# Optimization experiments

Measured on AMD Instinct MI355X. Metric: run time of the kernel, lower is better.

Reference implementation:

```python
import jax, jax.numpy as jnp
import numpy as np

B, T, C, H = 4, 2048, 768, 12
D = C // H

def setup_inputs() -> dict:
    key = jax.random.key(0)
    ks = jax.random.split(key, 8)
    s = 1.0 / np.sqrt(C)
    return {
        "x":  jax.random.normal(ks[0], (B, T, C), dtype=jnp.float32),
        "Wq": jax.random.normal(ks[1], (C, C), dtype=jnp.float32) * s,
        "bq": jax.random.normal(ks[2], (C,), dtype=jnp.float32) * 0.02,
        "Wk": jax.random.normal(ks[3], (C, C), dtype=jnp.float32) * s,
        "bk": jax.random.normal(ks[4], (C,), dtype=jnp.float32) * 0.02,
        "Wv": jax.random.normal(ks[5], (C, C), dtype=jnp.float32) * s,
        "bv": jax.random.normal(ks[6], (C,), dtype=jnp.float32) * 0.02,
        "Wp": jax.random.normal(ks[7], (C, C), dtype=jnp.float32) * s,
    }

def reference(x, Wq, bq, Wk, bk, Wv, bv, Wp):
    # Linear projections (torch Linear: y = x @ W.T + b)
    q = x @ Wq.T + bq
    k = x @ Wk.T + bk
    v = x @ Wv.T + bv
    # [B,T,C] -> [B,H,T,D]
    q = q.reshape(B, T, H, D).transpose(0, 2, 1, 3)
    k = k.reshape(B, T, H, D).transpose(0, 2, 1, 3)
    v = v.reshape(B, T, H, D).transpose(0, 2, 1, 3)
    scale = 1.0 / np.sqrt(D).astype(np.float32)
    scores = jnp.einsum('bhqd,bhkd->bhqk', q, k) * scale  # [B,H,T,T]
    attn = jax.nn.softmax(scores, axis=-1)  # no mask in original module
    out = jnp.einsum('bhqk,bhkd->bhqd', attn, v)
    out = out.transpose(0, 2, 1, 3).reshape(B, T, C)
    return out @ Wp.T  # proj has bias=False
```

## Files before the change

### kernel.cpp

```cpp
#include <hip/hip_runtime.h>
#include <hip/hip_bf16.h>
#include <cmath>

constexpr int B  = 4;
constexpr int T  = 2048;
constexpr int C  = 768;
constexpr int H  = 12;
constexpr int Dh = 64;
constexpr int M  = B * T;
constexpr int NQKV = 3 * C;
constexpr int WS2  = C * C;

typedef short bf16x8 __attribute__((ext_vector_type(8)));
typedef short bf16x4 __attribute__((ext_vector_type(4)));
typedef float f32x4  __attribute__((ext_vector_type(4)));

__device__ inline short f2bf(float f) {
    unsigned u = __float_as_uint(f);
    u += 0x7fffu + ((u >> 16) & 1u);
    return (short)(u >> 16);
}

__device__ inline unsigned pk_bf16(float a, float b) {
    __hip_bfloat162 h = __float22bfloat162_rn(float2{a, b});
    return *(unsigned*)&h;
}

typedef const __attribute__((address_space(1))) unsigned GU;
typedef __attribute__((address_space(3))) unsigned LU;
__device__ inline void async_copy16(const void* g, void* l) {
    __builtin_amdgcn_global_load_lds((GU*)g, (LU*)l, 16, 0, 0);
}

constexpr size_t XE = (size_t)M * C;
constexpr size_t CV_TOTAL = XE + 4 * (size_t)WS2;

__global__ __launch_bounds__(256)
void convert_all(const float* __restrict__ x,  const float* __restrict__ Wq,
                 const float* __restrict__ Wk, const float* __restrict__ Wv,
                 const float* __restrict__ Wp,
                 short* __restrict__ xb, short* __restrict__ Wqkv,
                 short* __restrict__ Wpb) {
    size_t i = ((size_t)blockIdx.x * 256 + threadIdx.x) * 4;
    const float* src; short* dst; size_t off;
    if (i < XE)                        { src = x;  dst = xb;            off = i; }
    else if (i < XE + WS2)             { src = Wq; dst = Wqkv;          off = i - XE; }
    else if (i < XE + 2 * (size_t)WS2) { src = Wk; dst = Wqkv + WS2;    off = i - XE - WS2; }
    else if (i < XE + 3 * (size_t)WS2) { src = Wv; dst = Wqkv + 2 * WS2; off = i - XE - 2 * (size_t)WS2; }
    else                               { src = Wp; dst = Wpb;           off = i - XE - 3 * (size_t)WS2; }
    float4 v = *(const float4*)(src + off);
    bf16x4 o; o[0] = f2bf(v.x); o[1] = f2bf(v.y); o[2] = f2bf(v.z); o[3] = f2bf(v.w);
    *(bf16x4*)(dst + off) = o;
}

constexpr int BM = 128;

template<int BN_, int WMW, int WNW, int OUT_BF16>
__global__ __launch_bounds__(256)
void gemm_bt(const short* __restrict__ A, const short* __restrict__ W,
             const float* __restrict__ bias0, const float* __restrict__ bias1,
             const float* __restrict__ bias2,
             void* __restrict__ Yv, int Ndim, int Kdim) {
    constexpr int MT  = BM / WMW / 16;
    constexpr int NT  = BN_ / WNW / 16;
    constexpr int NCH = (BM + BN_) / 16;

    __shared__ short As[2][BM * 32];
    __shared__ short Bs[2][BN_ * 32];

    const int tid  = threadIdx.x;
    const int wave = tid >> 6;
    const int lane = tid & 63;
    const int li   = lane & 15;
    const int quad = lane >> 4;
    const int wm   = wave % WMW;
    const int wn   = wave / WMW;
    const int m0   = blockIdx.y * BM;
    const int n0   = blockIdx.x * BN_;

    f32x4 acc[MT][NT];
    #pragma unroll
    for (int i = 0; i < MT; ++i)
        #pragma unroll
        for (int j = 0; j < NT; ++j)
            acc[i][j] = (f32x4){0.f, 0.f, 0.f, 0.f};

    const int lrow = lane >> 2;
    const int lkof = (lane & 3) * 8;

    auto stage = [&](int kk, int pbuf) {
        #pragma unroll
        for (int ii = 0; ii < NCH / 4; ++ii) {
            int c = ii * 4 + wave;
            if (c < BM / 16)
                async_copy16(A + (size_t)(m0 + c * 16 + lrow) * Kdim + kk + lkof,
                             &As[pbuf][c * 512]);
            else
                async_copy16(W + (size_t)(n0 + (c - BM / 16) * 16 + lrow) * Kdim + kk + lkof,
                             &Bs[pbuf][(c - BM / 16) * 512]);
        }
    };

    stage(0, 0);

    int pi = 0;
    for (int k0 = 0; k0 < Kdim; k0 += 32, pi ^= 1) {
        __syncthreads();
        if (k0 + 32 < Kdim) stage(k0 + 32, pi ^ 1);

        bf16x8 af[MT], bfr[NT];
        #pragma unroll
        for (int t = 0; t < MT; ++t)
            af[t] = *(const bf16x8*)&As[pi][(wm * MT * 16 + t * 16 + li) * 32 + quad * 8];
        #pragma unroll
        for (int t = 0; t < NT; ++t)
            bfr[t] = *(const bf16x8*)&Bs[pi][(wn * NT * 16 + t * 16 + li) * 32 + quad * 8];
        #pragma unroll
        for (int i = 0; i < MT; ++i)
            #pragma unroll
            for (int j = 0; j < NT; ++j)
                acc[i][j] = __builtin_amdgcn_mfma_f32_16x16x32_bf16(
                    af[i], bfr[j], acc[i][j], 0, 0, 0);
    }

    float bb[NT];
    #pragma unroll
    for (int nt = 0; nt < NT; ++nt) bb[nt] = 0.f;
    if (bias0) {
        int s = n0 / C;
        const float* bp = (s == 0) ? bias0 : ((s == 1) ? bias1 : bias2);
        int nb = n0 % C;
        #pragma unroll
        for (int nt = 0; nt < NT; ++nt)
            bb[nt] = bp[nb + wn * NT * 16 + nt * 16 + li];
    }

    #pragma unroll
    for (int mt = 0; mt < MT; ++mt)
        #pragma unroll
        for (int nt = 0; nt < NT; ++nt)
            #pragma unroll
            for (int r = 0; r < 4; ++r) {
                int row = m0 + wm * MT * 16 + mt * 16 + quad * 4 + r;
                int col = n0 + wn * NT * 16 + nt * 16 + li;
                float v = acc[mt][nt][r] + bb[nt];
                if constexpr (OUT_BF16)
                    ((short*)Yv)[(size_t)row * Ndim + col] = f2bf(v);
                else
                    ((float*)Yv)[(size_t)row * Ndim + col] = v;
            }
}

constexpr int QT    = 128;
constexpr int KTT   = 32;
constexpr int KHALF = T / 2;
constexpr int KSTR  = 72;
constexpr int VSTR  = 40;
constexpr int PSTR  = 40;
constexpr int QS    = NQKV;
constexpr float SOFT_SCALE = 0.18033688011112042f;

__global__ __launch_bounds__(256)
void attn_fwd(const short* __restrict__ QKV, float* __restrict__ Opart,
              float* __restrict__ Lpart) {
    __shared__ short Ks[KTT * KSTR];
    __shared__ short Vt[Dh * VSTR];
    __shared__ short Ps[4 * 32 * PSTR];

    const int tid  = threadIdx.x;
    const int wave = tid >> 6;
    const int lane = tid & 63;
    const int li   = lane & 15;
    const int quad = lane >> 4;
    const int half = blockIdx.z & 1;
    const int b    = blockIdx.z >> 1;
    const int h    = blockIdx.y;
    const int qw   = blockIdx.x * QT + wave * 32;
    const int kt0  = half * KHALF;

    const short* Qg = QKV + (size_t)(b * T) * QS + h * Dh;
    const short* Kg = QKV + (size_t)(b * T) * QS + C + h * Dh;
    const short* Vg = QKV + (size_t)(b * T) * QS + 2 * C + h * Dh;

    bf16x8 qf[2][2];
    #pragma unroll
    for (int qb = 0; qb < 2; ++qb)
        #pragma unroll
        for (int dh = 0; dh < 2; ++dh)
            qf[qb][dh] = *(const bf16x8*)(Qg + (size_t)(qw + qb * 16 + li) * QS
                                             + dh * 32 + quad * 8);

    bf16x8 ones;
    #pragma unroll
    for (int i = 0; i < 8; ++i) ones[i] = (short)0x3F80;

    f32x4 oacc[2][4];
    #pragma unroll
    for (int qb = 0; qb < 2; ++qb)
        #pragma unroll
        for (int db = 0; db < 4; ++db)
            oacc[qb][db] = (f32x4){0.f, 0.f, 0.f, 0.f};
    f32x4 lacc[2] = {(f32x4){0.f, 0.f, 0.f, 0.f}, (f32x4){0.f, 0.f, 0.f, 0.f}};

    const int ktok = tid >> 3;
    const int kch  = tid & 7;
    const int vd2  = (tid & 31) * 2;
    const int vg   = tid >> 5;

    int4 kpre;
    unsigned vpre[4];
    kpre = *(const int4*)(Kg + (size_t)(kt0 + ktok) * QS + kch * 8);
    #pragma unroll
    for (int t2 = 0; t2 < 4; ++t2)
        vpre[t2] = *(const unsigned*)(Vg + (size_t)(kt0 + vg * 4 + t2) * QS + vd2);

    for (int kt = kt0; kt < kt0 + KHALF; kt += KTT) {
        __syncthreads();

        *(int4*)&Ks[ktok * KSTR + kch * 8] = kpre;
        {
            unsigned lo0 = __builtin_amdgcn_perm(vpre[1], vpre[0], 0x05040100u);
            unsigned lo1 = __builtin_amdgcn_perm(vpre[3], vpre[2], 0x05040100u);
            unsigned hi0 = __builtin_amdgcn_perm(vpre[1], vpre[0], 0x07060302u);
            unsigned hi1 = __builtin_amdgcn_perm(vpre[3], vpre[2], 0x07060302u);
            *(uint2*)&Vt[vd2 * VSTR + vg * 4]       = make_uint2(lo0, lo1);
            *(uint2*)&Vt[(vd2 + 1) * VSTR + vg * 4] = make_uint2(hi0, hi1);
        }
        __syncthreads();

        if (kt + KTT < kt0 + KHALF) {
            const size_t nb = kt + KTT;
            kpre = *(const int4*)(Kg + (nb + ktok) * QS + kch * 8);
            #pragma unroll
            for (int t2 = 0; t2 < 4; ++t2)
                vpre[t2] = *(const unsigned*)(Vg + (nb + vg * 4 + t2) * QS + vd2);
        }

        f32x4 st[2][2];
        #pragma unroll
        for (int kb = 0; kb < 2; ++kb) {
            bf16x8 kf0 = *(const bf16x8*)&Ks[(kb * 16 + li) * KSTR + quad * 8];
            bf16x8 kf1 = *(const bf16x8*)&Ks[(kb * 16 + li) * KSTR + 32 + quad * 8];
            #pragma unroll
            for (int qb = 0; qb < 2; ++qb) {
                f32x4 a = (f32x4){0.f, 0.f, 0.f, 0.f};
                a = __builtin_amdgcn_mfma_f32_16x16x32_bf16(kf0, qf[qb][0], a, 0, 0, 0);
                a = __builtin_amdgcn_mfma_f32_16x16x32_bf16(kf1, qf[qb][1], a, 0, 0, 0);
                st[qb][kb] = a;
            }
        }

        #pragma unroll
        for (int qb = 0; qb < 2; ++qb)
            #pragma unroll
            for (int kb = 0; kb < 2; ++kb) {
                float p0 = __builtin_amdgcn_exp2f(st[qb][kb][0] * SOFT_SCALE);
                float p1 = __builtin_amdgcn_exp2f(st[qb][kb][1] * SOFT_SCALE);
                float p2 = __builtin_amdgcn_exp2f(st[qb][kb][2] * SOFT_SCALE);
                float p3 = __builtin_amdgcn_exp2f(st[qb][kb][3] * SOFT_SCALE);
                uint2 w; w.x = pk_bf16(p0, p1); w.y = pk_bf16(p2, p3);
                *(uint2*)&Ps[(wave * 32 + qb * 16 + li) * PSTR + kb * 16 + quad * 4] = w;
            }
        __asm__ volatile("s_waitcnt lgkmcnt(0)" ::: "memory");

        bf16x8 pf[2];
        #pragma unroll
        for (int qb = 0; qb < 2; ++qb) {
            pf[qb] = *(const bf16x8*)&Ps[(wave * 32 + qb * 16 + li) * PSTR + quad * 8];
            lacc[qb] = __builtin_amdgcn_mfma_f32_16x16x32_bf16(
                pf[qb], ones, lacc[qb], 0, 0, 0);
        }
        #pragma unroll
        for (int db = 0; db < 4; ++db) {
            bf16x8 vf = *(const bf16x8*)&Vt[(db * 16 + li) * VSTR + quad * 8];
            #pragma unroll
            for (int qb = 0; qb < 2; ++qb)
                oacc[qb][db] = __builtin_amdgcn_mfma_f32_16x16x32_bf16(
                    pf[qb], vf, oacc[qb][db], 0, 0, 0);
        }
    }

    float* Ob = Opart + (size_t)half * M * C;
    #pragma unroll
    for (int qb = 0; qb < 2; ++qb)
        #pragma unroll
        for (int r = 0; r < 4; ++r) {
            int row = qw + qb * 16 + quad * 4 + r;
            float* op = Ob + ((size_t)(b * T) + row) * C + h * Dh + li;
            #pragma unroll
            for (int db = 0; db < 4; ++db)
                op[db * 16] = oacc[qb][db][r];
            if (li == 0)
                Lpart[(size_t)half * M * H + ((size_t)(b * T) + row) * H + h]
                    = lacc[qb][r];
        }
}

__global__ __launch_bounds__(256)
void attn_reduce(const float* __restrict__ Op, const float* __restrict__ Lp,
                 short* __restrict__ AO) {
    int i = (blockIdx.x * 256 + threadIdx.x) * 8;
    int row = i / C;
    int col = i % C;
    int h = col >> 6;
    float l = Lp[(size_t)row * H + h] + Lp[(size_t)M * H + (size_t)row * H + h];
    float inv = 1.0f / l;
    const float* p0 = Op + i;
    const float* p1 = Op + (size_t)M * C + i;
    float4 a0 = *(const float4*)(p0);
    float4 a1 = *(const float4*)(p0 + 4);
    float4 b0 = *(const float4*)(p1);
    float4 b1 = *(const float4*)(p1 + 4);
    bf16x8 o;
    o[0] = f2bf((a0.x + b0.x) * inv); o[1] = f2bf((a0.y + b0.y) * inv);
    o[2] = f2bf((a0.z + b0.z) * inv); o[3] = f2bf((a0.w + b0.w) * inv);
    o[4] = f2bf((a1.x + b1.x) * inv); o[5] = f2bf((a1.y + b1.y) * inv);
    o[6] = f2bf((a1.z + b1.z) * inv); o[7] = f2bf((a1.w + b1.w) * inv);
    *(bf16x8*)(AO + i) = o;
}

extern "C" void kernel_launch(void* const* d_in, const int* in_sizes, int n_in,
                              void* d_out, int out_size, void* d_ws, size_t ws_size,
                              hipStream_t stream) {
    (void)in_sizes; (void)n_in; (void)out_size; (void)ws_size;

    const float* x  = (const float*)d_in[0];
    const float* Wq = (const float*)d_in[1];
    const float* bq = (const float*)d_in[2];
    const float* Wk = (const float*)d_in[3];
    const float* bk = (const float*)d_in[4];
    const float* Wv = (const float*)d_in[5];
    const float* bv = (const float*)d_in[6];
    const float* Wp = (const float*)d_in[7];
    float* out = (float*)d_out;

    short* xb    = (short*)d_ws;
    short* Wqkv  = xb + XE;
    short* Wpb   = Wqkv + 3 * (size_t)WS2;
    short* QKVb  = Wpb + (size_t)WS2;
    float* Opart = (float*)(QKVb + (size_t)M * NQKV);
    float* Lpart = (float*)Wqkv;
    short* AOb   = xb;

    convert_all<<<dim3(CV_TOTAL / 1024), 256, 0, stream>>>(
        x, Wq, Wk, Wv, Wp, xb, Wqkv, Wpb);

    gemm_bt<128, 2, 2, 1><<<dim3(NQKV / 128, M / BM), 256, 0, stream>>>(
        xb, Wqkv, bq, bk, bv, QKVb, NQKV, C);

    attn_fwd<<<dim3(T / QT, H, B * 2), 256, 0, stream>>>(QKVb, Opart, Lpart);

    attn_reduce<<<dim3((M * C) / 2048), 256, 0, stream>>>(Opart, Lpart, AOb);

    gemm_bt<64, 4, 1, 0><<<dim3(C / 64, M / BM), 256, 0, stream>>>(
        AOb, Wpb, nullptr, nullptr, nullptr, out, C, C);
}
```

Measured before the change: 250.1 us.

## Keep P in registers via 16x16x16 MFMA, sum rows in VALU, store partials as bf16

The attention kernel no longer writes the probability tile to LDS and reads it back. The exp outputs are packed directly into bf16x4 operands for 16x16x16 MFMAs against V, which removes the LDS round trip, the wait, and the ones-vector MFMA for row sums. Row sums are now accumulated in fp32 per lane and reduced with cross-lane shuffles. Partial outputs are stored as bf16 instead of fp32, halving partial-output traffic in both attention and reduce, at the cost of extra rounding error and twice as many smaller MFMAs.

```diff
diff --git a/kernel.cpp b/kernel.cpp
--- a/kernel.cpp
+++ b/kernel.cpp
@@ -156,16 +156,14 @@
 constexpr int KHALF = T / 2;
 constexpr int KSTR  = 72;
 constexpr int VSTR  = 40;
-constexpr int PSTR  = 40;
 constexpr int QS    = NQKV;
 constexpr float SOFT_SCALE = 0.18033688011112042f;
 
 __global__ __launch_bounds__(256)
-void attn_fwd(const short* __restrict__ QKV, float* __restrict__ Opart,
+void attn_fwd(const short* __restrict__ QKV, short* __restrict__ Opart,
               float* __restrict__ Lpart) {
     __shared__ short Ks[KTT * KSTR];
     __shared__ short Vt[Dh * VSTR];
-    __shared__ short Ps[4 * 32 * PSTR];
 
     const int tid  = threadIdx.x;
     const int wave = tid >> 6;
@@ -190,17 +188,13 @@
             qf[qb][dh] = *(const bf16x8*)(Qg + (size_t)(qw + qb * 16 + li) * QS
                                              + dh * 32 + quad * 8);
 
-    bf16x8 ones;
-    #pragma unroll
-    for (int i = 0; i < 8; ++i) ones[i] = (short)0x3F80;
-
     f32x4 oacc[2][4];
     #pragma unroll
     for (int qb = 0; qb < 2; ++qb)
         #pragma unroll
         for (int db = 0; db < 4; ++db)
             oacc[qb][db] = (f32x4){0.f, 0.f, 0.f, 0.f};
-    f32x4 lacc[2] = {(f32x4){0.f, 0.f, 0.f, 0.f}, (f32x4){0.f, 0.f, 0.f, 0.f}};
+    float lpart[2] = {0.f, 0.f};
 
     const int ktok = tid >> 3;
     const int kch  = tid & 7;
@@ -250,6 +244,7 @@
             }
         }
 
+        bf16x4 pf[2][2];
         #pragma unroll
         for (int qb = 0; qb < 2; ++qb)
             #pragma unroll
@@ -258,46 +253,55 @@
                 float p1 = __builtin_amdgcn_exp2f(st[qb][kb][1] * SOFT_SCALE);
                 float p2 = __builtin_amdgcn_exp2f(st[qb][kb][2] * SOFT_SCALE);
                 float p3 = __builtin_amdgcn_exp2f(st[qb][kb][3] * SOFT_SCALE);
-                uint2 w; w.x = pk_bf16(p0, p1); w.y = pk_bf16(p2, p3);
-                *(uint2*)&Ps[(wave * 32 + qb * 16 + li) * PSTR + kb * 16 + quad * 4] = w;
+                lpart[qb] += (p0 + p1) + (p2 + p3);
+                unsigned w0 = pk_bf16(p0, p1), w1 = pk_bf16(p2, p3);
+                uint2 packed = make_uint2(w0, w1);
+                pf[qb][kb] = *(bf16x4*)&packed;
             }
-        __asm__ volatile("s_waitcnt lgkmcnt(0)" ::: "memory");
-
-        bf16x8 pf[2];
-        #pragma unroll
-        for (int qb = 0; qb < 2; ++qb) {
-            pf[qb] = *(const bf16x8*)&Ps[(wave * 32 + qb * 16 + li) * PSTR + quad * 8];
-            lacc[qb] = __builtin_amdgcn_mfma_f32_16x16x32_bf16(
-                pf[qb], ones, lacc[qb], 0, 0, 0);
-        }
-        #pragma unroll
-        for (int db = 0; db < 4; ++db) {
-            bf16x8 vf = *(const bf16x8*)&Vt[(db * 16 + li) * VSTR + quad * 8];
-            #pragma unroll
-            for (int qb = 0; qb < 2; ++qb)
-                oacc[qb][db] = __builtin_amdgcn_mfma_f32_16x16x32_bf16(
-                    pf[qb], vf, oacc[qb][db], 0, 0, 0);
-        }
-    }
-
-    float* Ob = Opart + (size_t)half * M * C;
+
+        #pragma unroll
+        for (int kb = 0; kb < 2; ++kb)
+            #pragma unroll
+            for (int db = 0; db < 4; ++db) {
+                bf16x4 vf = *(const bf16x4*)&Vt[(db * 16 + li) * VSTR
+                                                + kb * 16 + quad * 4];
+                #pragma unroll
+                for (int qb = 0; qb < 2; ++qb)
+                    oacc[qb][db] = __builtin_amdgcn_mfma_f32_16x16x16bf16_1k(
+                        pf[qb][kb], vf, oacc[qb][db], 0, 0, 0);
+            }
+    }
+
+    float lq[2];
+    #pragma unroll
+    for (int qb = 0; qb < 2; ++qb) {
+        float v = lpart[qb];
+        v += __shfl_xor(v, 16);
+        v += __shfl_xor(v, 32);
+        lq[qb] = v;
+    }
+    if (quad == 0) {
+        #pragma unroll
+        for (int qb = 0; qb < 2; ++qb)
+            Lpart[(size_t)half * M * H + ((size_t)(b * T) + qw + qb * 16 + li) * H + h]
+                = lq[qb];
+    }
+
+    short* Ob = Opart + (size_t)half * M * C;
     #pragma unroll
     for (int qb = 0; qb < 2; ++qb)
         #pragma unroll
         for (int r = 0; r < 4; ++r) {
             int row = qw + qb * 16 + quad * 4 + r;
-            float* op = Ob + ((size_t)(b * T) + row) * C + h * Dh + li;
+            short* op = Ob + ((size_t)(b * T) + row) * C + h * Dh + li;
             #pragma unroll
             for (int db = 0; db < 4; ++db)
-                op[db * 16] = oacc[qb][db][r];
-            if (li == 0)
-                Lpart[(size_t)half * M * H + ((size_t)(b * T) + row) * H + h]
-                    = lacc[qb][r];
+                op[db * 16] = f2bf(oacc[qb][db][r]);
         }
 }
 
 __global__ __launch_bounds__(256)
-void attn_reduce(const float* __restrict__ Op, const float* __restrict__ Lp,
+void attn_reduce(const short* __restrict__ Op, const float* __restrict__ Lp,
                  short* __restrict__ AO) {
     int i = (blockIdx.x * 256 + threadIdx.x) * 8;
     int row = i / C;
@@ -305,17 +309,20 @@
     int h = col >> 6;
     float l = Lp[(size_t)row * H + h] + Lp[(size_t)M * H + (size_t)row * H + h];
     float inv = 1.0f / l;
-    const float* p0 = Op + i;
-    const float* p1 = Op + (size_t)M * C + i;
-    float4 a0 = *(const float4*)(p0);
-    float4 a1 = *(const float4*)(p0 + 4);
-    float4 b0 = *(const float4*)(p1);
-    float4 b1 = *(const float4*)(p1 + 4);
+    uint4 a = *(const uint4*)(Op + i);
+    uint4 bq = *(const uint4*)(Op + (size_t)M * C + i);
+    const unsigned* au = &a.x;
+    const unsigned* bu = &bq.x;
     bf16x8 o;
-    o[0] = f2bf((a0.x + b0.x) * inv); o[1] = f2bf((a0.y + b0.y) * inv);
-    o[2] = f2bf((a0.z + b0.z) * inv); o[3] = f2bf((a0.w + b0.w) * inv);
-    o[4] = f2bf((a1.x + b1.x) * inv); o[5] = f2bf((a1.y + b1.y) * inv);
-    o[6] = f2bf((a1.z + b1.z) * inv); o[7] = f2bf((a1.w + b1.w) * inv);
+    #pragma unroll
+    for (int j = 0; j < 4; ++j) {
+        float alo = __uint_as_float(au[j] << 16);
+        float ahi = __uint_as_float(au[j] & 0xffff0000u);
+        float blo = __uint_as_float(bu[j] << 16);
+        float bhi = __uint_as_float(bu[j] & 0xffff0000u);
+        o[2 * j]     = f2bf((alo + blo) * inv);
+        o[2 * j + 1] = f2bf((ahi + bhi) * inv);
+    }
     *(bf16x8*)(AO + i) = o;
 }
 
@@ -338,7 +345,7 @@
     short* Wqkv  = xb + XE;
     short* Wpb   = Wqkv + 3 * (size_t)WS2;
     short* QKVb  = Wpb + (size_t)WS2;
-    float* Opart = (float*)(QKVb + (size_t)M * NQKV);
+    short* Opart = QKVb + (size_t)M * NQKV;
     float* Lpart = (float*)Wqkv;
     short* AOb   = xb;
 
```

New measurement: 253.3 us. Within noise of the previous version (+1.3%).

## Use register-prefetch GEMM staging with BK=64 and bf16 attention partials

Applied to the files above, without the earlier changes.

The GEMM drops the async global-to-LDS double buffer. It now prefetches the next 64-wide K slice into registers, writes it to a single LDS buffer between two barriers, and runs two MFMA k-steps per tile. Separately, the split-K attention partial outputs are stored as bf16 instead of fp32, which halves the write and read traffic of the partials in attn_fwd and attn_reduce. The risks are more barriers per K step, more register pressure from the prefetch buffers, possible LDS bank conflicts with the unpadded 64-wide rows, and extra rounding error from bf16 partial sums.

```diff
diff --git a/kernel.cpp b/kernel.cpp
--- a/kernel.cpp
+++ b/kernel.cpp
@@ -24,12 +24,6 @@
 __device__ inline unsigned pk_bf16(float a, float b) {
     __hip_bfloat162 h = __float22bfloat162_rn(float2{a, b});
     return *(unsigned*)&h;
-}
-
-typedef const __attribute__((address_space(1))) unsigned GU;
-typedef __attribute__((address_space(3))) unsigned LU;
-__device__ inline void async_copy16(const void* g, void* l) {
-    __builtin_amdgcn_global_load_lds((GU*)g, (LU*)l, 16, 0, 0);
 }
 
 constexpr size_t XE = (size_t)M * C;
@@ -63,10 +57,11 @@
              void* __restrict__ Yv, int Ndim, int Kdim) {
     constexpr int MT  = BM / WMW / 16;
     constexpr int NT  = BN_ / WNW / 16;
-    constexpr int NCH = (BM + BN_) / 16;
-
-    __shared__ short As[2][BM * 32];
-    __shared__ short Bs[2][BN_ * 32];
+    constexpr int CHA = BM / 32;
+    constexpr int CHW = BN_ / 32;
+
+    __shared__ short As[BM * 64];
+    __shared__ short Bs[BN_ * 64];
 
     const int tid  = threadIdx.x;
     const int wave = tid >> 6;
@@ -85,42 +80,54 @@
         for (int j = 0; j < NT; ++j)
             acc[i][j] = (f32x4){0.f, 0.f, 0.f, 0.f};
 
-    const int lrow = lane >> 2;
-    const int lkof = (lane & 3) * 8;
-
-    auto stage = [&](int kk, int pbuf) {
-        #pragma unroll
-        for (int ii = 0; ii < NCH / 4; ++ii) {
-            int c = ii * 4 + wave;
-            if (c < BM / 16)
-                async_copy16(A + (size_t)(m0 + c * 16 + lrow) * Kdim + kk + lkof,
-                             &As[pbuf][c * 512]);
-            else
-                async_copy16(W + (size_t)(n0 + (c - BM / 16) * 16 + lrow) * Kdim + kk + lkof,
-                             &Bs[pbuf][(c - BM / 16) * 512]);
-        }
+    const int srow = tid >> 3;
+    const int sch  = (tid & 7) * 8;
+
+    const short* Abase = A + (size_t)(m0 + srow) * Kdim + sch;
+    const short* Wbase = W + (size_t)(n0 + srow) * Kdim + sch;
+
+    int4 pre[CHA + CHW];
+    auto prefetch = [&](int kk) {
+        #pragma unroll
+        for (int i = 0; i < CHA; ++i)
+            pre[i] = *(const int4*)(Abase + (size_t)i * 32 * Kdim + kk);
+        #pragma unroll
+        for (int i = 0; i < CHW; ++i)
+            pre[CHA + i] = *(const int4*)(Wbase + (size_t)i * 32 * Kdim + kk);
     };
-
-    stage(0, 0);
-
-    int pi = 0;
-    for (int k0 = 0; k0 < Kdim; k0 += 32, pi ^= 1) {
+    prefetch(0);
+
+    short* Adst = &As[srow * 64 + sch];
+    short* Wdst = &Bs[srow * 64 + sch];
+
+    for (int k0 = 0; k0 < Kdim; k0 += 64) {
         __syncthreads();
-        if (k0 + 32 < Kdim) stage(k0 + 32, pi ^ 1);
-
-        bf16x8 af[MT], bfr[NT];
-        #pragma unroll
-        for (int t = 0; t < MT; ++t)
-            af[t] = *(const bf16x8*)&As[pi][(wm * MT * 16 + t * 16 + li) * 32 + quad * 8];
-        #pragma unroll
-        for (int t = 0; t < NT; ++t)
-            bfr[t] = *(const bf16x8*)&Bs[pi][(wn * NT * 16 + t * 16 + li) * 32 + quad * 8];
-        #pragma unroll
-        for (int i = 0; i < MT; ++i)
-            #pragma unroll
-            for (int j = 0; j < NT; ++j)
-                acc[i][j] = __builtin_amdgcn_mfma_f32_16x16x32_bf16(
-                    af[i], bfr[j], acc[i][j], 0, 0, 0);
+        #pragma unroll
+        for (int i = 0; i < CHA; ++i) *(int4*)(Adst + i * 2048) = pre[i];
+        #pragma unroll
+        for (int i = 0; i < CHW; ++i) *(int4*)(Wdst + i * 2048) = pre[CHA + i];
+        __syncthreads();
+
+        if (k0 + 64 < Kdim) prefetch(k0 + 64);
+
+        #pragma unroll
+        for (int h = 0; h < 2; ++h) {
+            bf16x8 af[MT], bfr[NT];
+            #pragma unroll
+            for (int t = 0; t < MT; ++t)
+                af[t] = *(const bf16x8*)&As[(wm * MT * 16 + t * 16 + li) * 64
+                                            + h * 32 + quad * 8];
+            #pragma unroll
+            for (int t = 0; t < NT; ++t)
+                bfr[t] = *(const bf16x8*)&Bs[(wn * NT * 16 + t * 16 + li) * 64
+                                             + h * 32 + quad * 8];
+            #pragma unroll
+            for (int i = 0; i < MT; ++i)
+                #pragma unroll
+                for (int j = 0; j < NT; ++j)
+                    acc[i][j] = __builtin_amdgcn_mfma_f32_16x16x32_bf16(
+                        af[i], bfr[j], acc[i][j], 0, 0, 0);
+        }
     }
 
     float bb[NT];
@@ -161,7 +168,7 @@
 constexpr float SOFT_SCALE = 0.18033688011112042f;
 
 __global__ __launch_bounds__(256)
-void attn_fwd(const short* __restrict__ QKV, float* __restrict__ Opart,
+void attn_fwd(const short* __restrict__ QKV, short* __restrict__ Opart,
               float* __restrict__ Lpart) {
     __shared__ short Ks[KTT * KSTR];
     __shared__ short Vt[Dh * VSTR];
@@ -280,16 +287,16 @@
         }
     }
 
-    float* Ob = Opart + (size_t)half * M * C;
+    short* Ob = Opart + (size_t)half * M * C;
     #pragma unroll
     for (int qb = 0; qb < 2; ++qb)
         #pragma unroll
         for (int r = 0; r < 4; ++r) {
             int row = qw + qb * 16 + quad * 4 + r;
-            float* op = Ob + ((size_t)(b * T) + row) * C + h * Dh + li;
+            short* op = Ob + ((size_t)(b * T) + row) * C + h * Dh + li;
             #pragma unroll
             for (int db = 0; db < 4; ++db)
-                op[db * 16] = oacc[qb][db][r];
+                op[db * 16] = f2bf(oacc[qb][db][r]);
             if (li == 0)
                 Lpart[(size_t)half * M * H + ((size_t)(b * T) + row) * H + h]
                     = lacc[qb][r];
@@ -297,7 +304,7 @@
 }
 
 __global__ __launch_bounds__(256)
-void attn_reduce(const float* __restrict__ Op, const float* __restrict__ Lp,
+void attn_reduce(const short* __restrict__ Op, const float* __restrict__ Lp,
                  short* __restrict__ AO) {
     int i = (blockIdx.x * 256 + threadIdx.x) * 8;
     int row = i / C;
@@ -305,17 +312,20 @@
     int h = col >> 6;
     float l = Lp[(size_t)row * H + h] + Lp[(size_t)M * H + (size_t)row * H + h];
     float inv = 1.0f / l;
-    const float* p0 = Op + i;
-    const float* p1 = Op + (size_t)M * C + i;
-    float4 a0 = *(const float4*)(p0);
-    float4 a1 = *(const float4*)(p0 + 4);
-    float4 b0 = *(const float4*)(p1);
-    float4 b1 = *(const float4*)(p1 + 4);
+    uint4 a = *(const uint4*)(Op + i);
+    uint4 bq = *(const uint4*)(Op + (size_t)M * C + i);
+    const unsigned* au = &a.x;
+    const unsigned* bu = &bq.x;
     bf16x8 o;
-    o[0] = f2bf((a0.x + b0.x) * inv); o[1] = f2bf((a0.y + b0.y) * inv);
-    o[2] = f2bf((a0.z + b0.z) * inv); o[3] = f2bf((a0.w + b0.w) * inv);
-    o[4] = f2bf((a1.x + b1.x) * inv); o[5] = f2bf((a1.y + b1.y) * inv);
-    o[6] = f2bf((a1.z + b1.z) * inv); o[7] = f2bf((a1.w + b1.w) * inv);
+    #pragma unroll
+    for (int j = 0; j < 4; ++j) {
+        float alo = __uint_as_float(au[j] << 16);
+        float ahi = __uint_as_float(au[j] & 0xffff0000u);
+        float blo = __uint_as_float(bu[j] << 16);
+        float bhi = __uint_as_float(bu[j] & 0xffff0000u);
+        o[2 * j]     = f2bf((alo + blo) * inv);
+        o[2 * j + 1] = f2bf((ahi + bhi) * inv);
+    }
     *(bf16x8*)(AO + i) = o;
 }
 
@@ -338,7 +348,7 @@
     short* Wqkv  = xb + XE;
     short* Wpb   = Wqkv + 3 * (size_t)WS2;
     short* QKVb  = Wpb + (size_t)WS2;
-    float* Opart = (float*)(QKVb + (size_t)M * NQKV);
+    short* Opart = QKVb + (size_t)M * NQKV;
     float* Lpart = (float*)Wqkv;
     short* AOb   = xb;
 
```

Result: slower. 382.5 us (+52.9%).

## Split attention keys four ways and store partial outputs in bf16

Applied to the files above, without the earlier changes.

The attention kernel now splits the key dimension into four chunks instead of two, which doubles the number of blocks to improve occupancy and tail balance. Partial outputs are written as bf16 instead of fp32, so total partial-output traffic and workspace stay about the same despite the extra splits. The reduce kernel sums four bf16 partials and four row-sum partials. Rounding partials to bf16 before summing adds some numerical error.

```diff
diff --git a/kernel.cpp b/kernel.cpp
--- a/kernel.cpp
+++ b/kernel.cpp
@@ -153,7 +153,8 @@
 
 constexpr int QT    = 128;
 constexpr int KTT   = 32;
-constexpr int KHALF = T / 2;
+constexpr int NSPLIT = 4;
+constexpr int KHALF = T / NSPLIT;
 constexpr int KSTR  = 72;
 constexpr int VSTR  = 40;
 constexpr int PSTR  = 40;
@@ -161,7 +162,7 @@
 constexpr float SOFT_SCALE = 0.18033688011112042f;
 
 __global__ __launch_bounds__(256)
-void attn_fwd(const short* __restrict__ QKV, float* __restrict__ Opart,
+void attn_fwd(const short* __restrict__ QKV, short* __restrict__ Opart,
               float* __restrict__ Lpart) {
     __shared__ short Ks[KTT * KSTR];
     __shared__ short Vt[Dh * VSTR];
@@ -172,8 +173,8 @@
     const int lane = tid & 63;
     const int li   = lane & 15;
     const int quad = lane >> 4;
-    const int half = blockIdx.z & 1;
-    const int b    = blockIdx.z >> 1;
+    const int half = blockIdx.z & (NSPLIT - 1);
+    const int b    = blockIdx.z >> 2;
     const int h    = blockIdx.y;
     const int qw   = blockIdx.x * QT + wave * 32;
     const int kt0  = half * KHALF;
@@ -280,16 +281,16 @@
         }
     }
 
-    float* Ob = Opart + (size_t)half * M * C;
+    short* Ob = Opart + (size_t)half * M * C;
     #pragma unroll
     for (int qb = 0; qb < 2; ++qb)
         #pragma unroll
         for (int r = 0; r < 4; ++r) {
             int row = qw + qb * 16 + quad * 4 + r;
-            float* op = Ob + ((size_t)(b * T) + row) * C + h * Dh + li;
+            short* op = Ob + ((size_t)(b * T) + row) * C + h * Dh + li;
             #pragma unroll
             for (int db = 0; db < 4; ++db)
-                op[db * 16] = oacc[qb][db][r];
+                op[db * 16] = f2bf(oacc[qb][db][r]);
             if (li == 0)
                 Lpart[(size_t)half * M * H + ((size_t)(b * T) + row) * H + h]
                     = lacc[qb][r];
@@ -297,25 +298,32 @@
 }
 
 __global__ __launch_bounds__(256)
-void attn_reduce(const float* __restrict__ Op, const float* __restrict__ Lp,
+void attn_reduce(const short* __restrict__ Op, const float* __restrict__ Lp,
                  short* __restrict__ AO) {
     int i = (blockIdx.x * 256 + threadIdx.x) * 8;
     int row = i / C;
     int col = i % C;
     int h = col >> 6;
-    float l = Lp[(size_t)row * H + h] + Lp[(size_t)M * H + (size_t)row * H + h];
+    float l = 0.f;
+    #pragma unroll
+    for (int s = 0; s < NSPLIT; ++s)
+        l += Lp[(size_t)s * M * H + (size_t)row * H + h];
     float inv = 1.0f / l;
-    const float* p0 = Op + i;
-    const float* p1 = Op + (size_t)M * C + i;
-    float4 a0 = *(const float4*)(p0);
-    float4 a1 = *(const float4*)(p0 + 4);
-    float4 b0 = *(const float4*)(p1);
-    float4 b1 = *(const float4*)(p1 + 4);
+
+    float sum[8] = {};
+    #pragma unroll
+    for (int s = 0; s < NSPLIT; ++s) {
+        uint4 a = *(const uint4*)(Op + (size_t)s * M * C + i);
+        const unsigned* au = &a.x;
+        #pragma unroll
+        for (int j = 0; j < 4; ++j) {
+            sum[2 * j]     += __uint_as_float(au[j] << 16);
+            sum[2 * j + 1] += __uint_as_float(au[j] & 0xffff0000u);
+        }
+    }
     bf16x8 o;
-    o[0] = f2bf((a0.x + b0.x) * inv); o[1] = f2bf((a0.y + b0.y) * inv);
-    o[2] = f2bf((a0.z + b0.z) * inv); o[3] = f2bf((a0.w + b0.w) * inv);
-    o[4] = f2bf((a1.x + b1.x) * inv); o[5] = f2bf((a1.y + b1.y) * inv);
-    o[6] = f2bf((a1.z + b1.z) * inv); o[7] = f2bf((a1.w + b1.w) * inv);
+    #pragma unroll
+    for (int j = 0; j < 8; ++j) o[j] = f2bf(sum[j] * inv);
     *(bf16x8*)(AO + i) = o;
 }
 
@@ -338,7 +346,7 @@
     short* Wqkv  = xb + XE;
     short* Wpb   = Wqkv + 3 * (size_t)WS2;
     short* QKVb  = Wpb + (size_t)WS2;
-    float* Opart = (float*)(QKVb + (size_t)M * NQKV);
+    short* Opart = QKVb + (size_t)M * NQKV;
     float* Lpart = (float*)Wqkv;
     short* AOb   = xb;
 
@@ -348,7 +356,7 @@
     gemm_bt<128, 2, 2, 1><<<dim3(NQKV / 128, M / BM), 256, 0, stream>>>(
         xb, Wqkv, bq, bk, bv, QKVb, NQKV, C);
 
-    attn_fwd<<<dim3(T / QT, H, B * 2), 256, 0, stream>>>(QKVb, Opart, Lpart);
+    attn_fwd<<<dim3(T / QT, H, B * NSPLIT), 256, 0, stream>>>(QKVb, Opart, Lpart);
 
     attn_reduce<<<dim3((M * C) / 2048), 256, 0, stream>>>(Opart, Lpart, AOb);
 
```

After: 250.4 us. Within noise of the previous version (+0.1%).
